# Kernel tuning notes

Hardware: AMD Instinct MI355X
Metric: run time of the kernel (lower is better)

## Reference

```python
import jax, jax.numpy as jnp
import numpy as np

N = 100000      # nodes
E = 1600000     # edges (avg degree 16)
IN = 128        # input_dim
HID = 32        # hidden_dim per head (layer 1)
HEADS = 2       # heads (layer 1)
OUT = 32        # output_dim (layer 2, heads=1)
NEG_SLOPE = 0.2 # PyG GATConv default leaky relu slope


def setup_inputs() -> dict:
    key = jax.random.key(0)
    ks = jax.random.split(key, 10)
    s = 0.1  # glorot-ish scale
    x = jax.random.normal(ks[0], (N, IN), jnp.float32)
    edge_index = jax.random.randint(ks[1], (2, E), 0, N, dtype=jnp.int64)
    W1 = jax.random.normal(ks[2], (IN, HEADS * HID), jnp.float32) * s
    a1_src = jax.random.normal(ks[3], (HEADS, HID), jnp.float32) * s
    a1_dst = jax.random.normal(ks[4], (HEADS, HID), jnp.float32) * s
    b1 = jnp.zeros((HEADS * HID,), jnp.float32)
    W2 = jax.random.normal(ks[5], (HEADS * HID, OUT), jnp.float32) * s
    a2_src = jax.random.normal(ks[6], (1, OUT), jnp.float32) * s
    a2_dst = jax.random.normal(ks[7], (1, OUT), jnp.float32) * s
    b2 = jnp.zeros((OUT,), jnp.float32)
    return {"x": x, "edge_index": edge_index, "W1": W1, "a1_src": a1_src,
            "a1_dst": a1_dst, "b1": b1, "W2": W2, "a2_src": a2_src,
            "a2_dst": a2_dst, "b2": b2}


def _gat_layer(x, src, dst, W, a_src, a_dst, b, heads, out_ch, concat, n_nodes):
    # linear projection: [N, heads, out_ch]
    h = (x @ W).reshape(n_nodes, heads, out_ch)
    # per-node attention halves: [N, heads]
    alpha_s = jnp.einsum('nhc,hc->nh', h, a_src)
    alpha_d = jnp.einsum('nhc,hc->nh', h, a_dst)
    # per-edge raw score (message x_j = source node, softmax over dst segment)
    e = jax.nn.leaky_relu(alpha_s[src] + alpha_d[dst], NEG_SLOPE)  # [E, heads]
    # segment softmax over incoming edges of each dst node
    m = jax.ops.segment_max(e, dst, num_segments=n_nodes)          # [N, heads]
    m = jax.lax.stop_gradient(m)
    ee = jnp.exp(e - m[dst])
    denom = jax.ops.segment_sum(ee, dst, num_segments=n_nodes)     # [N, heads]
    alpha = ee / (denom[dst] + 1e-16)                              # [E, heads]
    # weighted scatter-add aggregation
    msg = h[src] * alpha[:, :, None]                               # [E, heads, out_ch]
    out = jax.ops.segment_sum(msg, dst, num_segments=n_nodes)      # [N, heads, out_ch]
    if concat:
        out = out.reshape(n_nodes, heads * out_ch)
    else:
        out = out.mean(axis=1)
    return out + b


def reference(x, edge_index, W1, a1_src, a1_dst, b1, W2, a2_src, a2_dst, b2):
    n = x.shape[0]
    # PyG GATConv adds self-loops by default (both layers, same edge set)
    loop = jnp.arange(n, dtype=edge_index.dtype)
    src = jnp.concatenate([edge_index[0], loop])
    dst = jnp.concatenate([edge_index[1], loop])
    h = _gat_layer(x, src, dst, W1, a1_src, a1_dst, b1, HEADS, HID, True, n)
    h = jax.nn.elu(h)
    return _gat_layer(h, src, dst, W2, a2_src, a2_dst, b2, 1, OUT, False, n)
```

## Files before the change

kernel.cpp:

```cpp
#include <hip/hip_runtime.h>
#include <math.h>

#define N_NODES 100000
#define N_EDGES 1600000
#define IN_DIM  128
#define C1      64
#define OUT_DIM 32
#define NEG_SLOPE 0.2f
#define LOG2E 1.44269504f

#define BSHIFT  8
#define BNODES  256
#define NBUCK   ((N_NODES + BNODES - 1) / BNODES)
#define CAP     5120
#define SLOTS   48
#define GC_STRIDE 16
#define G1_BLOCKS ((N_NODES + 127) / 128)

typedef _Float16 half8 __attribute__((ext_vector_type(8)));
typedef float    f32x4 __attribute__((ext_vector_type(4)));

__device__ __forceinline__ float wexp2(float sc) {
    return __builtin_amdgcn_exp2f(fmaxf(sc, NEG_SLOPE * sc));
}


__global__ void zero_k(int4* __restrict__ p, int n4) {
    int i = blockIdx.x * 256 + threadIdx.x;
    if (i < n4) p[i] = make_int4(0, 0, 0, 0);
}

__global__ __launch_bounds__(1024) void binp1_k(const int* __restrict__ ei,
        int* __restrict__ gcur, int* __restrict__ buf) {
    __shared__ int scnt[NBUCK], sbase[NBUCK], soff[NBUCK];
    int t = threadIdx.x;
    if (t < NBUCK) { scnt[t] = 0; soff[t] = 0; }
    __syncthreads();
    int  s[16], bk[16], ld[16];
    bool v[16];
    #pragma unroll
    for (int i = 0; i < 16; ++i) {
        int e = blockIdx.x * 16384 + i * 1024 + t;
        v[i] = e < N_EDGES;
        int ec = v[i] ? e : 0;
        s[i] = ei[ec];
        int d = ei[N_EDGES + ec];
        bk[i] = d >> BSHIFT;
        ld[i] = d & (BNODES - 1);
        if (v[i]) atomicAdd(&scnt[bk[i]], 1);
    }
    __syncthreads();
    if (t < NBUCK) sbase[t] = atomicAdd(&gcur[t * GC_STRIDE], scnt[t]);
    __syncthreads();
    #pragma unroll
    for (int i = 0; i < 16; ++i) {
        if (v[i]) {
            int p = sbase[bk[i]] + atomicAdd(&soff[bk[i]], 1);
            if (p < CAP) buf[bk[i] * CAP + p] = s[i] | (ld[i] << 17);
        }
    }
}

__global__ __launch_bounds__(256) void binp2_k(const int* __restrict__ gcur,
        const int* __restrict__ buf, int* __restrict__ csr, int* __restrict__ deg) {
    __shared__ int4 lcsr4[BNODES * SLOTS / 4];
    __shared__ int  lcnt[BNODES];
    int* lcsr = (int*)lcsr4;
    int b = blockIdx.x, t = threadIdx.x;
    lcnt[t] = 0;
    __syncthreads();
    int cnt = gcur[b * GC_STRIDE];
    if (cnt > CAP) cnt = CAP;
    const int* bb = buf + b * CAP;
    for (int e = t; e < cnt; e += 256) {
        int vv = bb[e];
        int src = vv & 0x1FFFF;
        int l = vv >> 17;
        int slot = atomicAdd(&lcnt[l], 1);
        if (slot < SLOTS) lcsr[l * SLOTS + slot] = src;
    }
    __syncthreads();
    int4* g4 = (int4*)csr + (size_t)b * (BNODES * SLOTS / 4);
    #pragma unroll
    for (int i = 0; i < BNODES * SLOTS / 4 / 256; ++i)
        g4[t + i * 256] = lcsr4[t + i * 256];
    int c = lcnt[t];
    deg[b * BNODES + t] = c < SLOTS ? c : SLOTS;
}

__global__ void prep_k(const float* __restrict__ W1, const float* __restrict__ W2,
                       _Float16* __restrict__ w1t, _Float16* __restrict__ w2t) {
    int t = blockIdx.x * 256 + threadIdx.x;
    if (t < IN_DIM * C1) {
        int k = t >> 6, n = t & 63;
        w1t[n * IN_DIM + k] = (_Float16)W1[t];
    }
    if (t < C1 * OUT_DIM) {
        int k = t >> 5, n = t & 31;
        w2t[n * C1 + k] = (_Float16)W2[t];
    }
}

__global__ __launch_bounds__(256) void gemm1_k(const float* __restrict__ x,
        const _Float16* __restrict__ w1t, const float* __restrict__ a_s,
        const float* __restrict__ a_d, _Float16* __restrict__ h,
        float* __restrict__ as_o, float* __restrict__ ad_o) {
    __shared__ _Float16 sh[4][32 * 72];
    int t = threadIdx.x;
    int wv = t >> 6, lane = t & 63, m = lane & 15, q = lane >> 4;
    int rbw = blockIdx.x * 128 + wv * 32;
    f32x4 acc[2][4];
    #pragma unroll
    for (int i = 0; i < 2; ++i)
        #pragma unroll
        for (int j = 0; j < 4; ++j) acc[i][j] = (f32x4){0.f, 0.f, 0.f, 0.f};
    #pragma unroll
    for (int ks = 0; ks < 4; ++ks) {
        half8 a[2];
        #pragma unroll
        for (int rt = 0; rt < 2; ++rt) {
            int r = rbw + rt * 16 + m;
            r = r < N_NODES ? r : 0;
            const float4* p = (const float4*)(x + (size_t)r * IN_DIM + ks * 32 + q * 8);
            float4 f0 = p[0], f1 = p[1];
            half8 av;
            av[0] = (_Float16)f0.x; av[1] = (_Float16)f0.y;
            av[2] = (_Float16)f0.z; av[3] = (_Float16)f0.w;
            av[4] = (_Float16)f1.x; av[5] = (_Float16)f1.y;
            av[6] = (_Float16)f1.z; av[7] = (_Float16)f1.w;
            a[rt] = av;
        }
        #pragma unroll
        for (int ct = 0; ct < 4; ++ct) {
            half8 b = *(const half8*)(w1t + (ct * 16 + m) * IN_DIM + ks * 32 + q * 8);
            acc[0][ct] = __builtin_amdgcn_mfma_f32_16x16x32_f16(a[0], b, acc[0][ct], 0, 0, 0);
            acc[1][ct] = __builtin_amdgcn_mfma_f32_16x16x32_f16(a[1], b, acc[1][ct], 0, 0, 0);
        }
    }
    _Float16* ws = sh[wv];
    #pragma unroll
    for (int rt = 0; rt < 2; ++rt)
        #pragma unroll
        for (int ct = 0; ct < 4; ++ct)
            #pragma unroll
            for (int r = 0; r < 4; ++r)
                ws[(rt * 16 + q * 4 + r) * 72 + ct * 16 + m] = (_Float16)acc[rt][ct][r];
    __syncthreads();
    int rl = lane >> 1, hp = lane & 1;
    int rg = rbw + rl;
    if (rg < N_NODES) {
        float As_r[32], Ad_r[32];
        const float4* ap = (const float4*)(a_s + hp * 32);
        const float4* dp = (const float4*)(a_d + hp * 32);
        #pragma unroll
        for (int i = 0; i < 8; ++i) {
            float4 v = ap[i];
            As_r[4*i] = v.x; As_r[4*i+1] = v.y; As_r[4*i+2] = v.z; As_r[4*i+3] = v.w;
            float4 u = dp[i];
            Ad_r[4*i] = u.x; Ad_r[4*i+1] = u.y; Ad_r[4*i+2] = u.z; Ad_r[4*i+3] = u.w;
        }
        const _Float16* rowp = ws + rl * 72 + hp * 32;
        half8 c0 = *(const half8*)(rowp);
        half8 c1 = *(const half8*)(rowp + 8);
        half8 c2 = *(const half8*)(rowp + 16);
        half8 c3 = *(const half8*)(rowp + 24);
        float s = 0.f, dd = 0.f;
        #pragma unroll
        for (int j = 0; j < 8; ++j) {
            s  = fmaf((float)c0[j], As_r[j],      s);
            dd = fmaf((float)c0[j], Ad_r[j],      dd);
            s  = fmaf((float)c1[j], As_r[8 + j],  s);
            dd = fmaf((float)c1[j], Ad_r[8 + j],  dd);
            s  = fmaf((float)c2[j], As_r[16 + j], s);
            dd = fmaf((float)c2[j], Ad_r[16 + j], dd);
            s  = fmaf((float)c3[j], As_r[24 + j], s);
            dd = fmaf((float)c3[j], Ad_r[24 + j], dd);
        }
        as_o[rg * 2 + hp] = s  * LOG2E;
        ad_o[rg * 2 + hp] = dd * LOG2E;
        _Float16* hr = h + (size_t)rg * C1 + hp * 32;
        *(half8*)(hr)      = c0;
        *(half8*)(hr + 8)  = c1;
        *(half8*)(hr + 16) = c2;
        *(half8*)(hr + 24) = c3;
    }
}

__global__ __launch_bounds__(256) void gemm2_k(const _Float16* __restrict__ xh,
        const _Float16* __restrict__ w2t, const float* __restrict__ a_s,
        const float* __restrict__ a_d, _Float16* __restrict__ h,
        float* __restrict__ as_o, float* __restrict__ ad_o) {
    __shared__ _Float16 sh[4][32 * 36];
    int t = threadIdx.x;
    int wv = t >> 6, lane = t & 63, m = lane & 15, q = lane >> 4;
    int rbw = blockIdx.x * 128 + wv * 32;
    f32x4 acc[2][2];
    #pragma unroll
    for (int i = 0; i < 2; ++i)
        #pragma unroll
        for (int j = 0; j < 2; ++j) acc[i][j] = (f32x4){0.f, 0.f, 0.f, 0.f};
    #pragma unroll
    for (int ks = 0; ks < 2; ++ks) {
        half8 a[2];
        #pragma unroll
        for (int rt = 0; rt < 2; ++rt) {
            int r = rbw + rt * 16 + m;
            r = r < N_NODES ? r : 0;
            a[rt] = *(const half8*)(xh + (size_t)r * C1 + ks * 32 + q * 8);
        }
        #pragma unroll
        for (int ct = 0; ct < 2; ++ct) {
            half8 b = *(const half8*)(w2t + (ct * 16 + m) * C1 + ks * 32 + q * 8);
            acc[0][ct] = __builtin_amdgcn_mfma_f32_16x16x32_f16(a[0], b, acc[0][ct], 0, 0, 0);
            acc[1][ct] = __builtin_amdgcn_mfma_f32_16x16x32_f16(a[1], b, acc[1][ct], 0, 0, 0);
        }
    }
    _Float16* ws = sh[wv];
    #pragma unroll
    for (int rt = 0; rt < 2; ++rt)
        #pragma unroll
        for (int ct = 0; ct < 2; ++ct)
            #pragma unroll
            for (int r = 0; r < 4; ++r)
                ws[(rt * 16 + q * 4 + r) * 36 + ct * 16 + m] = (_Float16)acc[rt][ct][r];
    __syncthreads();
    if (lane < 32) {
        int rg = rbw + lane;
        if (rg < N_NODES) {
            float As_r[32], Ad_r[32];
            const float4* ap = (const float4*)a_s;
            const float4* dp = (const float4*)a_d;
            #pragma unroll
            for (int i = 0; i < 8; ++i) {
                float4 v = ap[i];
                As_r[4*i] = v.x; As_r[4*i+1] = v.y; As_r[4*i+2] = v.z; As_r[4*i+3] = v.w;
                float4 u = dp[i];
                Ad_r[4*i] = u.x; Ad_r[4*i+1] = u.y; Ad_r[4*i+2] = u.z; Ad_r[4*i+3] = u.w;
            }
            const _Float16* rowp = ws + lane * 36;
            half8 c0 = *(const half8*)(rowp);
            half8 c1 = *(const half8*)(rowp + 8);
            half8 c2 = *(const half8*)(rowp + 16);
            half8 c3 = *(const half8*)(rowp + 24);
            float s = 0.f, dd = 0.f;
            #pragma unroll
            for (int j = 0; j < 8; ++j) {
                s  = fmaf((float)c0[j], As_r[j],      s);
                dd = fmaf((float)c0[j], Ad_r[j],      dd);
                s  = fmaf((float)c1[j], As_r[8 + j],  s);
                dd = fmaf((float)c1[j], Ad_r[8 + j],  dd);
                s  = fmaf((float)c2[j], As_r[16 + j], s);
                dd = fmaf((float)c2[j], Ad_r[16 + j], dd);
                s  = fmaf((float)c3[j], As_r[24 + j], s);
                dd = fmaf((float)c3[j], Ad_r[24 + j], dd);
            }
            as_o[rg] = s  * LOG2E;
            ad_o[rg] = dd * LOG2E;
            _Float16* hr = h + (size_t)rg * OUT_DIM;
            *(half8*)(hr)      = c0;
            *(half8*)(hr + 8)  = c1;
            *(half8*)(hr + 16) = c2;
            *(half8*)(hr + 24) = c3;
        }
    }
}


__global__ __launch_bounds__(256) void agg1_k(const int* __restrict__ deg,
        const int* __restrict__ csr, const _Float16* __restrict__ h1,
        const float* __restrict__ as1, const float* __restrict__ ad1,
        const float* __restrict__ b1, _Float16* __restrict__ helu) {
    int lane = threadIdx.x & 63;
    int dl   = lane >> 4;
    int eg   = (lane >> 3) & 1;
    int cl   = lane & 7;
    int head = cl >> 2;
    int d = ((blockIdx.x * 256 + threadIdx.x) >> 6) * 4 + dl;
    int cnt = deg[d];
    const int* row = csr + d * SLOTS;
    float advl = ad1[d * 2 + head];
    float acc[8] = {0.f, 0.f, 0.f, 0.f, 0.f, 0.f, 0.f, 0.f};
    float wsum = 0.f;
    for (int base = 0; base < cnt; base += 4) {
        int e0 = base + eg, e1 = base + 2 + eg;
        bool v0 = e0 < cnt, v1 = e1 < cnt;
        int s0 = row[v0 ? e0 : 0];
        int s1 = row[v1 ? e1 : 0];
        float a0 = as1[s0 * 2 + head];
        float a1 = as1[s1 * 2 + head];
        half8 g0 = *(const half8*)(h1 + (size_t)s0 * C1 + 8 * cl);
        half8 g1 = *(const half8*)(h1 + (size_t)s1 * C1 + 8 * cl);
        float w0 = v0 ? wexp2(a0 + advl) : 0.f;
        float w1 = v1 ? wexp2(a1 + advl) : 0.f;
        #pragma unroll
        for (int i = 0; i < 8; ++i) {
            acc[i] = fmaf((float)g0[i], w0, acc[i]);
            acc[i] = fmaf((float)g1[i], w1, acc[i]);
        }
        wsum += w0 + w1;
    }
    if (eg == 0) {
        float w = wexp2(as1[d * 2 + head] + advl);
        half8 g = *(const half8*)(h1 + (size_t)d * C1 + 8 * cl);
        #pragma unroll
        for (int i = 0; i < 8; ++i) acc[i] = fmaf((float)g[i], w, acc[i]);
        wsum += w;
    }
    #pragma unroll
    for (int i = 0; i < 8; ++i) acc[i] += __shfl_xor(acc[i], 8);
    wsum += __shfl_xor(wsum, 8);
    if (eg == 0) {
        float inv = 1.f / (wsum + 1e-16f);
        const float4* bv = (const float4*)(b1 + 8 * cl);
        float o[8];
        #pragma unroll
        for (int i = 0; i < 4; ++i) {
            o[i]     = acc[i]     * inv + (&bv[0].x)[i];
            o[4 + i] = acc[4 + i] * inv + (&bv[1].x)[i];
        }
        half8 hv;
        #pragma unroll
        for (int i = 0; i < 8; ++i) {
            float e = o[i] > 0.f ? o[i] : __expf(o[i]) - 1.f;
            hv[i] = (_Float16)e;
        }
        *(half8*)(helu + (size_t)d * C1 + 8 * cl) = hv;
    }
}

__global__ __launch_bounds__(256) void agg2_k(const int* __restrict__ deg,
        const int* __restrict__ csr, const _Float16* __restrict__ h2,
        const float* __restrict__ as2, const float* __restrict__ ad2,
        const float* __restrict__ b2, float* __restrict__ out) {
    int lane = threadIdx.x & 63;
    int dl   = lane >> 3;
    int eg   = (lane >> 2) & 1;
    int cl   = lane & 3;
    int d = ((blockIdx.x * 256 + threadIdx.x) >> 6) * 8 + dl;
    int cnt = deg[d];
    const int* row = csr + d * SLOTS;
    float advl = ad2[d];
    float acc[8] = {0.f, 0.f, 0.f, 0.f, 0.f, 0.f, 0.f, 0.f};
    float wsum = 0.f;
    for (int base = 0; base < cnt; base += 4) {
        int e0 = base + eg, e1 = base + 2 + eg;
        bool v0 = e0 < cnt, v1 = e1 < cnt;
        int s0 = row[v0 ? e0 : 0];
        int s1 = row[v1 ? e1 : 0];
        float a0 = as2[s0];
        float a1 = as2[s1];
        half8 g0 = *(const half8*)(h2 + (size_t)s0 * OUT_DIM + 8 * cl);
        half8 g1 = *(const half8*)(h2 + (size_t)s1 * OUT_DIM + 8 * cl);
        float w0 = v0 ? wexp2(a0 + advl) : 0.f;
        float w1 = v1 ? wexp2(a1 + advl) : 0.f;
        #pragma unroll
        for (int i = 0; i < 8; ++i) {
            acc[i] = fmaf((float)g0[i], w0, acc[i]);
            acc[i] = fmaf((float)g1[i], w1, acc[i]);
        }
        wsum += w0 + w1;
    }
    if (eg == 0) {
        float w = wexp2(as2[d] + advl);
        half8 g = *(const half8*)(h2 + (size_t)d * OUT_DIM + 8 * cl);
        #pragma unroll
        for (int i = 0; i < 8; ++i) acc[i] = fmaf((float)g[i], w, acc[i]);
        wsum += w;
    }
    #pragma unroll
    for (int i = 0; i < 8; ++i) acc[i] += __shfl_xor(acc[i], 4);
    wsum += __shfl_xor(wsum, 4);
    if (eg == 0) {
        float inv = 1.f / (wsum + 1e-16f);
        const float4* bv = (const float4*)(b2 + 8 * cl);
        float4 o0, o1;
        o0.x = acc[0] * inv + bv[0].x; o0.y = acc[1] * inv + bv[0].y;
        o0.z = acc[2] * inv + bv[0].z; o0.w = acc[3] * inv + bv[0].w;
        o1.x = acc[4] * inv + bv[1].x; o1.y = acc[5] * inv + bv[1].y;
        o1.z = acc[6] * inv + bv[1].z; o1.w = acc[7] * inv + bv[1].w;
        float4* ow = (float4*)(out + (size_t)d * OUT_DIM + 8 * cl);
        ow[0] = o0;
        ow[1] = o1;
    }
}


extern "C" void kernel_launch(void* const* d_in, const int* in_sizes, int n_in,
                              void* d_out, int out_size, void* d_ws, size_t ws_size,
                              hipStream_t stream) {
    const float* x   = (const float*)d_in[0];
    const int*   ei  = (const int*)d_in[1];
    const float* W1  = (const float*)d_in[2];
    const float* a1s = (const float*)d_in[3];
    const float* a1d = (const float*)d_in[4];
    const float* b1  = (const float*)d_in[5];
    const float* W2  = (const float*)d_in[6];
    const float* a2s = (const float*)d_in[7];
    const float* a2d = (const float*)d_in[8];
    const float* b2  = (const float*)d_in[9];
    float* out = (float*)d_out;

    char* ws = (char*)d_ws;
    size_t off = 0;
    auto alloc = [&](size_t bytes) -> void* {
        void* p = ws + off;
        off = (off + bytes + 255) & ~(size_t)255;
        return p;
    };
    int* gcur      = (int*)alloc((size_t)NBUCK * GC_STRIDE * 4);
    int* buf       = (int*)alloc((size_t)NBUCK * CAP * 4);
    int* csr       = (int*)alloc((size_t)NBUCK * BNODES * SLOTS * 4);
    int* deg       = (int*)alloc((size_t)NBUCK * BNODES * 4);
    _Float16* w1t  = (_Float16*)alloc((size_t)IN_DIM * C1 * 2);
    _Float16* w2t  = (_Float16*)alloc((size_t)C1 * OUT_DIM * 2);
    _Float16* h1   = (_Float16*)alloc((size_t)N_NODES * C1 * 2);
    float* as1     = (float*)alloc((size_t)N_NODES * 2 * 4);
    float* ad1     = (float*)alloc((size_t)N_NODES * 2 * 4);
    _Float16* helu = (_Float16*)alloc((size_t)N_NODES * C1 * 2);
    _Float16* h2   = (_Float16*)alloc((size_t)N_NODES * OUT_DIM * 2);
    float* as2     = (float*)alloc((size_t)N_NODES * 4);
    float* ad2     = (float*)alloc((size_t)N_NODES * 4);

    const int ZN4 = NBUCK * GC_STRIDE / 4;
    zero_k<<<(ZN4 + 255) / 256, 256, 0, stream>>>((int4*)gcur, ZN4);
    binp1_k<<<(N_EDGES + 16383) / 16384, 1024, 0, stream>>>(ei, gcur, buf);
    binp2_k<<<NBUCK, 256, 0, stream>>>(gcur, buf, csr, deg);
    prep_k<<<(IN_DIM * C1 + 255) / 256, 256, 0, stream>>>(W1, W2, w1t, w2t);

    gemm1_k<<<G1_BLOCKS, 256, 0, stream>>>(x, w1t, a1s, a1d, h1, as1, ad1);
    agg1_k<<<N_NODES / 16, 256, 0, stream>>>(deg, csr, h1, as1, ad1, b1, helu);
    gemm2_k<<<G1_BLOCKS, 256, 0, stream>>>(helu, w2t, a2s, a2d, h2, as2, ad2);
    agg2_k<<<N_NODES / 32, 256, 0, stream>>>(deg, csr, h2, as2, ad2, b2, out);
}
```

Baseline: 228.5 us.

## Fuse layer-2 projection GEMM into layer-1 aggregation kernel via shared memory

```diff
diff --git a/kernel.cpp b/kernel.cpp
--- a/kernel.cpp
+++ b/kernel.cpp
@@ -186,96 +186,24 @@
     }
 }
 
-__global__ __launch_bounds__(256) void gemm2_k(const _Float16* __restrict__ xh,
-        const _Float16* __restrict__ w2t, const float* __restrict__ a_s,
-        const float* __restrict__ a_d, _Float16* __restrict__ h,
-        float* __restrict__ as_o, float* __restrict__ ad_o) {
-    __shared__ _Float16 sh[4][32 * 36];
-    int t = threadIdx.x;
-    int wv = t >> 6, lane = t & 63, m = lane & 15, q = lane >> 4;
-    int rbw = blockIdx.x * 128 + wv * 32;
-    f32x4 acc[2][2];
-    #pragma unroll
-    for (int i = 0; i < 2; ++i)
-        #pragma unroll
-        for (int j = 0; j < 2; ++j) acc[i][j] = (f32x4){0.f, 0.f, 0.f, 0.f};
-    #pragma unroll
-    for (int ks = 0; ks < 2; ++ks) {
-        half8 a[2];
-        #pragma unroll
-        for (int rt = 0; rt < 2; ++rt) {
-            int r = rbw + rt * 16 + m;
-            r = r < N_NODES ? r : 0;
-            a[rt] = *(const half8*)(xh + (size_t)r * C1 + ks * 32 + q * 8);
-        }
-        #pragma unroll
-        for (int ct = 0; ct < 2; ++ct) {
-            half8 b = *(const half8*)(w2t + (ct * 16 + m) * C1 + ks * 32 + q * 8);
-            acc[0][ct] = __builtin_amdgcn_mfma_f32_16x16x32_f16(a[0], b, acc[0][ct], 0, 0, 0);
-            acc[1][ct] = __builtin_amdgcn_mfma_f32_16x16x32_f16(a[1], b, acc[1][ct], 0, 0, 0);
-        }
-    }
-    _Float16* ws = sh[wv];
-    #pragma unroll
-    for (int rt = 0; rt < 2; ++rt)
-        #pragma unroll
-        for (int ct = 0; ct < 2; ++ct)
-            #pragma unroll
-            for (int r = 0; r < 4; ++r)
-                ws[(rt * 16 + q * 4 + r) * 36 + ct * 16 + m] = (_Float16)acc[rt][ct][r];
-    __syncthreads();
-    if (lane < 32) {
-        int rg = rbw + lane;
-        if (rg < N_NODES) {
-            float As_r[32], Ad_r[32];
-            const float4* ap = (const float4*)a_s;
-            const float4* dp = (const float4*)a_d;
-            #pragma unroll
-            for (int i = 0; i < 8; ++i) {
-                float4 v = ap[i];
-                As_r[4*i] = v.x; As_r[4*i+1] = v.y; As_r[4*i+2] = v.z; As_r[4*i+3] = v.w;
-                float4 u = dp[i];
-                Ad_r[4*i] = u.x; Ad_r[4*i+1] = u.y; Ad_r[4*i+2] = u.z; Ad_r[4*i+3] = u.w;
-            }
-            const _Float16* rowp = ws + lane * 36;
-            half8 c0 = *(const half8*)(rowp);
-            half8 c1 = *(const half8*)(rowp + 8);
-            half8 c2 = *(const half8*)(rowp + 16);
-            half8 c3 = *(const half8*)(rowp + 24);
-            float s = 0.f, dd = 0.f;
-            #pragma unroll
-            for (int j = 0; j < 8; ++j) {
-                s  = fmaf((float)c0[j], As_r[j],      s);
-                dd = fmaf((float)c0[j], Ad_r[j],      dd);
-                s  = fmaf((float)c1[j], As_r[8 + j],  s);
-                dd = fmaf((float)c1[j], Ad_r[8 + j],  dd);
-                s  = fmaf((float)c2[j], As_r[16 + j], s);
-                dd = fmaf((float)c2[j], Ad_r[16 + j], dd);
-                s  = fmaf((float)c3[j], As_r[24 + j], s);
-                dd = fmaf((float)c3[j], Ad_r[24 + j], dd);
-            }
-            as_o[rg] = s  * LOG2E;
-            ad_o[rg] = dd * LOG2E;
-            _Float16* hr = h + (size_t)rg * OUT_DIM;
-            *(half8*)(hr)      = c0;
-            *(half8*)(hr + 8)  = c1;
-            *(half8*)(hr + 16) = c2;
-            *(half8*)(hr + 24) = c3;
-        }
-    }
-}
-
-
-__global__ __launch_bounds__(256) void agg1_k(const int* __restrict__ deg,
+__global__ __launch_bounds__(256) void agg1g2_k(const int* __restrict__ deg,
         const int* __restrict__ csr, const _Float16* __restrict__ h1,
         const float* __restrict__ as1, const float* __restrict__ ad1,
-        const float* __restrict__ b1, _Float16* __restrict__ helu) {
-    int lane = threadIdx.x & 63;
+        const float* __restrict__ b1, const _Float16* __restrict__ w2t,
+        const float* __restrict__ a2s, const float* __restrict__ a2d,
+        _Float16* __restrict__ h2, float* __restrict__ as2o,
+        float* __restrict__ ad2o) {
+    __shared__ _Float16 shu[16 * 72];
+    __shared__ _Float16 sh2[16 * 36];
+    int t = threadIdx.x;
+    int wv = t >> 6, lane = t & 63;
     int dl   = lane >> 4;
     int eg   = (lane >> 3) & 1;
     int cl   = lane & 7;
     int head = cl >> 2;
-    int d = ((blockIdx.x * 256 + threadIdx.x) >> 6) * 4 + dl;
+    int lr   = wv * 4 + dl;
+    int d    = blockIdx.x * 16 + lr;
+
     int cnt = deg[d];
     const int* row = csr + d * SLOTS;
     float advl = ad1[d * 2 + head];
@@ -286,10 +214,10 @@
         bool v0 = e0 < cnt, v1 = e1 < cnt;
         int s0 = row[v0 ? e0 : 0];
         int s1 = row[v1 ? e1 : 0];
-        float a0 = as1[s0 * 2 + head];
-        float a1 = as1[s1 * 2 + head];
-        half8 g0 = *(const half8*)(h1 + (size_t)s0 * C1 + 8 * cl);
-        half8 g1 = *(const half8*)(h1 + (size_t)s1 * C1 + 8 * cl);
+        float a0 = as1[(unsigned)(s0 * 2 + head)];
+        float a1 = as1[(unsigned)(s1 * 2 + head)];
+        half8 g0 = *(const half8*)(h1 + (unsigned)(s0 * C1 + 8 * cl));
+        half8 g1 = *(const half8*)(h1 + (unsigned)(s1 * C1 + 8 * cl));
         float w0 = v0 ? wexp2(a0 + advl) : 0.f;
         float w1 = v1 ? wexp2(a1 + advl) : 0.f;
         #pragma unroll
@@ -301,7 +229,7 @@
     }
     if (eg == 0) {
         float w = wexp2(as1[d * 2 + head] + advl);
-        half8 g = *(const half8*)(h1 + (size_t)d * C1 + 8 * cl);
+        half8 g = *(const half8*)(h1 + (unsigned)(d * C1 + 8 * cl));
         #pragma unroll
         for (int i = 0; i < 8; ++i) acc[i] = fmaf((float)g[i], w, acc[i]);
         wsum += w;
@@ -324,7 +252,68 @@
             float e = o[i] > 0.f ? o[i] : __expf(o[i]) - 1.f;
             hv[i] = (_Float16)e;
         }
-        *(half8*)(helu + (size_t)d * C1 + 8 * cl) = hv;
+        *(half8*)(shu + lr * 72 + cl * 8) = hv;
+    }
+    __syncthreads();
+
+    if (wv == 0) {
+        int m = lane & 15, q = lane >> 4;
+        f32x4 c2[2];
+        c2[0] = (f32x4){0.f, 0.f, 0.f, 0.f};
+        c2[1] = (f32x4){0.f, 0.f, 0.f, 0.f};
+        #pragma unroll
+        for (int ks = 0; ks < 2; ++ks) {
+            half8 a = *(const half8*)(shu + m * 72 + ks * 32 + q * 8);
+            #pragma unroll
+            for (int ct = 0; ct < 2; ++ct) {
+                half8 b = *(const half8*)(w2t + (ct * 16 + m) * C1 + ks * 32 + q * 8);
+                c2[ct] = __builtin_amdgcn_mfma_f32_16x16x32_f16(a, b, c2[ct], 0, 0, 0);
+            }
+        }
+        #pragma unroll
+        for (int ct = 0; ct < 2; ++ct)
+            #pragma unroll
+            for (int r = 0; r < 4; ++r)
+                sh2[(q * 4 + r) * 36 + ct * 16 + m] = (_Float16)c2[ct][r];
+    }
+    __syncthreads();
+
+    if (wv == 0 && lane < 16) {
+        int rg = blockIdx.x * 16 + lane;
+        float As_r[32], Ad_r[32];
+        const float4* ap = (const float4*)a2s;
+        const float4* dp = (const float4*)a2d;
+        #pragma unroll
+        for (int i = 0; i < 8; ++i) {
+            float4 v = ap[i];
+            As_r[4*i] = v.x; As_r[4*i+1] = v.y; As_r[4*i+2] = v.z; As_r[4*i+3] = v.w;
+            float4 u = dp[i];
+            Ad_r[4*i] = u.x; Ad_r[4*i+1] = u.y; Ad_r[4*i+2] = u.z; Ad_r[4*i+3] = u.w;
+        }
+        const _Float16* rowp = sh2 + lane * 36;
+        half8 c0 = *(const half8*)(rowp);
+        half8 c1 = *(const half8*)(rowp + 8);
+        half8 c2 = *(const half8*)(rowp + 16);
+        half8 c3 = *(const half8*)(rowp + 24);
+        float s = 0.f, dd = 0.f;
+        #pragma unroll
+        for (int j = 0; j < 8; ++j) {
+            s  = fmaf((float)c0[j], As_r[j],      s);
+            dd = fmaf((float)c0[j], Ad_r[j],      dd);
+            s  = fmaf((float)c1[j], As_r[8 + j],  s);
+            dd = fmaf((float)c1[j], Ad_r[8 + j],  dd);
+            s  = fmaf((float)c2[j], As_r[16 + j], s);
+            dd = fmaf((float)c2[j], Ad_r[16 + j], dd);
+            s  = fmaf((float)c3[j], As_r[24 + j], s);
+            dd = fmaf((float)c3[j], Ad_r[24 + j], dd);
+        }
+        as2o[rg] = s  * LOG2E;
+        ad2o[rg] = dd * LOG2E;
+        _Float16* hr = h2 + (size_t)rg * OUT_DIM;
+        *(half8*)(hr)      = c0;
+        *(half8*)(hr + 8)  = c1;
+        *(half8*)(hr + 16) = c2;
+        *(half8*)(hr + 24) = c3;
     }
 }
 
@@ -347,10 +336,10 @@
         bool v0 = e0 < cnt, v1 = e1 < cnt;
         int s0 = row[v0 ? e0 : 0];
         int s1 = row[v1 ? e1 : 0];
-        float a0 = as2[s0];
-        float a1 = as2[s1];
-        half8 g0 = *(const half8*)(h2 + (size_t)s0 * OUT_DIM + 8 * cl);
-        half8 g1 = *(const half8*)(h2 + (size_t)s1 * OUT_DIM + 8 * cl);
+        float a0 = as2[(unsigned)s0];
+        float a1 = as2[(unsigned)s1];
+        half8 g0 = *(const half8*)(h2 + (unsigned)(s0 * OUT_DIM + 8 * cl));
+        half8 g1 = *(const half8*)(h2 + (unsigned)(s1 * OUT_DIM + 8 * cl));
         float w0 = v0 ? wexp2(a0 + advl) : 0.f;
         float w1 = v1 ? wexp2(a1 + advl) : 0.f;
         #pragma unroll
@@ -362,7 +351,7 @@
     }
     if (eg == 0) {
         float w = wexp2(as2[d] + advl);
-        half8 g = *(const half8*)(h2 + (size_t)d * OUT_DIM + 8 * cl);
+        half8 g = *(const half8*)(h2 + (unsigned)(d * OUT_DIM + 8 * cl));
         #pragma unroll
         for (int i = 0; i < 8; ++i) acc[i] = fmaf((float)g[i], w, acc[i]);
         wsum += w;
@@ -416,7 +405,6 @@
     _Float16* h1   = (_Float16*)alloc((size_t)N_NODES * C1 * 2);
     float* as1     = (float*)alloc((size_t)N_NODES * 2 * 4);
     float* ad1     = (float*)alloc((size_t)N_NODES * 2 * 4);
-    _Float16* helu = (_Float16*)alloc((size_t)N_NODES * C1 * 2);
     _Float16* h2   = (_Float16*)alloc((size_t)N_NODES * OUT_DIM * 2);
     float* as2     = (float*)alloc((size_t)N_NODES * 4);
     float* ad2     = (float*)alloc((size_t)N_NODES * 4);
@@ -428,7 +416,7 @@
     prep_k<<<(IN_DIM * C1 + 255) / 256, 256, 0, stream>>>(W1, W2, w1t, w2t);
 
     gemm1_k<<<G1_BLOCKS, 256, 0, stream>>>(x, w1t, a1s, a1d, h1, as1, ad1);
-    agg1_k<<<N_NODES / 16, 256, 0, stream>>>(deg, csr, h1, as1, ad1, b1, helu);
-    gemm2_k<<<G1_BLOCKS, 256, 0, stream>>>(helu, w2t, a2s, a2d, h2, as2, ad2);
+    agg1g2_k<<<N_NODES / 16, 256, 0, stream>>>(deg, csr, h1, as1, ad1, b1,
+                                               w2t, a2s, a2d, h2, as2, ad2);
     agg2_k<<<N_NODES / 32, 256, 0, stream>>>(deg, csr, h2, as2, ad2, b2, out);
 }
```

Result: no change. 225.1 us (-1.4%).
